# Optimization experiments

Hardware: AMD Instinct MI355X
Metric: run time of the kernel (lower is better)

The kernel has to match this reference:

```python
import jax, jax.numpy as jnp
import numpy as np

HIDDEN = 1024
NUM_CLASSES = 10
NUM_GAUSSIANS = 8
IN_FEATURES = 16
HEADS = NUM_CLASSES * NUM_GAUSSIANS * IN_FEATURES * 2  # 2560 tiny Linear(hidden,1) heads


def setup_inputs() -> dict:
    key = jax.random.key(0)
    kx, kw, kb = jax.random.split(key, 3)
    x = jax.random.normal(kx, (8192, HIDDEN), dtype=jnp.float32)
    # Stacked weights of the 2560 per-head Linear(hidden,1) layers.
    bound = 1.0 / np.sqrt(HIDDEN)
    W = jax.random.uniform(kw, (HIDDEN, HEADS), minval=-bound, maxval=bound, dtype=jnp.float32)
    b = jax.random.uniform(kb, (HEADS,), minval=-bound, maxval=bound, dtype=jnp.float32)
    return {"x": x, "W": W, "b": b}


def reference(x, W, b):
    batch = x.shape[0]
    # Fused form of the Python loop of Linear(hidden,1)+Sigmoid per head.
    z = jax.nn.sigmoid(x @ W + b)  # [batch, HEADS]
    return z.reshape(batch, NUM_CLASSES, NUM_GAUSSIANS, IN_FEATURES, 2)
```

## Files before the change

### kernel.cpp

```cpp
#include <hip/hip_runtime.h>
#include <hip/hip_bf16.h>

#define HIDDEN 1024
#define HEADS  2560

#define BM 256
#define BN 128
#define BK 32
#define NT (HIDDEN / BK)
#define ABYT (BM * BK * 2)
#define BBYT (BN * BK * 2)
#define BUFSZ (ABYT + BBYT)

typedef float  f32x4  __attribute__((ext_vector_type(4)));
typedef __bf16 bf16x8 __attribute__((ext_vector_type(8)));
typedef __bf16 bf16x4 __attribute__((ext_vector_type(4)));

__device__ __forceinline__ void gload_lds16(const void* g, void* l) {
    __builtin_amdgcn_global_load_lds(
        (const __attribute__((address_space(1))) unsigned int*)g,
        (__attribute__((address_space(3))) unsigned int*)l, 16, 0, 0);
}
__device__ __forceinline__ unsigned swz(unsigned x) {
    return x ^ (((x >> 6) & 3u) << 4);
}

__global__ __launch_bounds__(256)
void cvt_all(const float* __restrict__ x, const float* __restrict__ W,
             __bf16* __restrict__ xc, __bf16* __restrict__ Wt, int n8)
{
    if (blockIdx.x < 640) {
        __shared__ __bf16 tile[64][72];
        const int t  = threadIdx.x;
        const int n0 = (blockIdx.x % 40) * 64;
        const int k0 = (blockIdx.x / 40) * 64;

        #pragma unroll
        for (int i = 0; i < 4; ++i) {
            const int k    = (t >> 4) + i * 16;
            const int col4 = (t & 15) * 4;
            const float4 v = *reinterpret_cast<const float4*>(
                W + (size_t)(k0 + k) * HEADS + n0 + col4);
            bf16x4 h;
            h[0] = (__bf16)v.x; h[1] = (__bf16)v.y; h[2] = (__bf16)v.z; h[3] = (__bf16)v.w;
            *reinterpret_cast<bf16x4*>(&tile[k][col4]) = h;
        }
        __syncthreads();
        #pragma unroll
        for (int i = 0; i < 4; ++i) {
            const int n  = (t >> 4) + i * 16;
            const int k4 = (t & 15) * 4;
            bf16x4 h;
            h[0] = tile[k4 + 0][n]; h[1] = tile[k4 + 1][n];
            h[2] = tile[k4 + 2][n]; h[3] = tile[k4 + 3][n];
            *reinterpret_cast<bf16x4*>(Wt + (size_t)(n0 + n) * HIDDEN + k0 + k4) = h;
        }
    } else {
        int idx    = (blockIdx.x - 640) * blockDim.x + threadIdx.x;
        int stride = (gridDim.x - 640) * blockDim.x;
        for (int i = idx; i < n8; i += stride) {
            const float4 a = *reinterpret_cast<const float4*>(x + (size_t)i * 8);
            const float4 b = *reinterpret_cast<const float4*>(x + (size_t)i * 8 + 4);
            bf16x8 h;
            h[0] = (__bf16)a.x; h[1] = (__bf16)a.y; h[2] = (__bf16)a.z; h[3] = (__bf16)a.w;
            h[4] = (__bf16)b.x; h[5] = (__bf16)b.y; h[6] = (__bf16)b.z; h[7] = (__bf16)b.w;
            *reinterpret_cast<bf16x8*>(xc + (size_t)i * 8) = h;
        }
    }
}

__global__ __launch_bounds__(512, 4)
void gemm_sq(const __bf16* __restrict__ A, const __bf16* __restrict__ Bt,
             const float* __restrict__ bias, float* __restrict__ out)
{
    __shared__ char lds[2 * BUFSZ];

    const int t    = threadIdx.x;
    const int lane = t & 63;
    const int w    = t >> 6;
    const int wr   = w & 3;
    const int wc   = w >> 2;
    const int lhi  = lane >> 4;
    const int llo  = lane & 15;

    const int g   = (blockIdx.x & 7) * 80 + (blockIdx.x >> 3);
    const int bx  = g / 20;
    const int by  = g % 20;
    const int bm0 = bx * BM;
    const int bn0 = by * BN;

    const unsigned d0 = (unsigned)(t * 16);
    const unsigned r0 = d0 >> 6;
    const unsigned c0 = (d0 & 63) ^ ((r0 & 3u) << 4);
    const char* asrc0 = (const char*)A  + (size_t)(bm0 + r0) * (HIDDEN * 2) + c0;
    const char* bsrc0 = (const char*)Bt + (size_t)(bn0 + r0) * (HIDDEN * 2) + c0;
    char* adst0 = (char*)lds + d0;
    char* bdst0 = (char*)lds + ABYT + d0;

    const unsigned klo  = ((unsigned)(lhi * 16)) ^ ((unsigned)((llo & 3) << 4));
    const unsigned rowA = (unsigned)((wr * 64 + llo) * 64);
    const unsigned rowB = (unsigned)ABYT + (unsigned)((wc * 64 + llo) * 64);

    f32x4 acc[4][4];
    #pragma unroll
    for (int m = 0; m < 4; ++m)
        #pragma unroll
        for (int n = 0; n < 4; ++n)
            acc[m][n] = f32x4{0.f, 0.f, 0.f, 0.f};

    gload_lds16(asrc0,          adst0);
    gload_lds16(asrc0 + 262144, adst0 + 8192);
    gload_lds16(bsrc0,          bdst0);
    asm volatile("s_waitcnt vmcnt(0)" ::: "memory");
    __builtin_amdgcn_s_barrier();

    for (int k = 0; k < NT; ++k) {
        const char* buf  = lds + (k & 1) * BUFSZ;
        const unsigned nb = (unsigned)(((k + 1) & 1) * BUFSZ);
        const int   koff = (k + 1) * 64;

        if (k + 1 < NT) {
            gload_lds16(asrc0 + koff,          adst0 + nb);
            gload_lds16(asrc0 + koff + 262144, adst0 + nb + 8192);
            gload_lds16(bsrc0 + koff,          bdst0 + nb);
        }

        bf16x8 af[4], bfr[4];
        #pragma unroll
        for (int m = 0; m < 4; ++m)
            af[m]  = *(const bf16x8*)(buf + rowA + m * 1024 + klo);
        #pragma unroll
        for (int n = 0; n < 4; ++n)
            bfr[n] = *(const bf16x8*)(buf + rowB + n * 1024 + klo);
        #pragma unroll
        for (int m = 0; m < 4; ++m)
            #pragma unroll
            for (int n = 0; n < 4; ++n)
                acc[m][n] = __builtin_amdgcn_mfma_f32_16x16x32_bf16(
                    af[m], bfr[n], acc[m][n], 0, 0, 0);

        asm volatile("s_waitcnt vmcnt(0)" ::: "memory");
        __builtin_amdgcn_s_barrier();
    }

    #pragma unroll
    for (int n = 0; n < 4; ++n) {
        const int col  = bn0 + wc * 64 + n * 16 + llo;
        const float bv = bias[col];
        #pragma unroll
        for (int m = 0; m < 4; ++m) {
            const int row0 = bm0 + wr * 64 + m * 16 + lhi * 4;
            #pragma unroll
            for (int r = 0; r < 4; ++r) {
                const float z = acc[m][n][r] + bv;
                out[(size_t)(row0 + r) * HEADS + col] = __fdividef(1.0f, 1.0f + __expf(-z));
            }
        }
    }
}

#define FBM 128
#define FBN 128
#define FBK 32
#define FLDK 40

__global__ __launch_bounds__(256)
void lch_gemm(const float* __restrict__ x, const float* __restrict__ W,
              const float* __restrict__ b, float* __restrict__ out)
{
    __shared__ __bf16 As[FBM][FLDK];
    __shared__ __bf16 Bs[FBN][FLDK];

    const int t   = threadIdx.x;
    const int bm0 = blockIdx.x * FBM;
    const int bn0 = blockIdx.y * FBN;
    const int lane = t & 63;
    const int wid  = t >> 6;
    const int wr   = wid >> 1;
    const int wc   = wid & 1;
    const int lhi  = lane >> 4;
    const int llo  = lane & 15;

    f32x4 acc[4][4];
    #pragma unroll
    for (int i = 0; i < 4; ++i)
        #pragma unroll
        for (int j = 0; j < 4; ++j)
            acc[i][j] = f32x4{0.f, 0.f, 0.f, 0.f};

    const int bn_col  = t & 127;
    const int bk_base = (t >> 7) * 16;

    for (int k0 = 0; k0 < HIDDEN; k0 += FBK) {
        #pragma unroll
        for (int i = 0; i < 4; ++i) {
            const int f   = t + i * 256;
            const int row = f >> 3;
            const int c4  = (f & 7) * 4;
            const float4 v = *reinterpret_cast<const float4*>(
                x + (size_t)(bm0 + row) * HIDDEN + k0 + c4);
            bf16x4 h;
            h[0] = (__bf16)v.x; h[1] = (__bf16)v.y;
            h[2] = (__bf16)v.z; h[3] = (__bf16)v.w;
            *reinterpret_cast<bf16x4*>(&As[row][c4]) = h;
        }
        {
            const float* wp = W + (size_t)(k0 + bk_base) * HEADS + bn0 + bn_col;
            bf16x8 h0, h1;
            #pragma unroll
            for (int i = 0; i < 8; ++i) h0[i] = (__bf16)wp[(size_t)i * HEADS];
            #pragma unroll
            for (int i = 0; i < 8; ++i) h1[i] = (__bf16)wp[(size_t)(i + 8) * HEADS];
            *reinterpret_cast<bf16x8*>(&Bs[bn_col][bk_base])     = h0;
            *reinterpret_cast<bf16x8*>(&Bs[bn_col][bk_base + 8]) = h1;
        }
        __syncthreads();

        bf16x8 af[4], bfr[4];
        #pragma unroll
        for (int i = 0; i < 4; ++i)
            af[i] = *reinterpret_cast<const bf16x8*>(&As[wr * 64 + i * 16 + llo][lhi * 8]);
        #pragma unroll
        for (int j = 0; j < 4; ++j)
            bfr[j] = *reinterpret_cast<const bf16x8*>(&Bs[wc * 64 + j * 16 + llo][lhi * 8]);
        #pragma unroll
        for (int i = 0; i < 4; ++i)
            #pragma unroll
            for (int j = 0; j < 4; ++j)
                acc[i][j] = __builtin_amdgcn_mfma_f32_16x16x32_bf16(
                    af[i], bfr[j], acc[i][j], 0, 0, 0);
        __syncthreads();
    }

    #pragma unroll
    for (int j = 0; j < 4; ++j) {
        const int col  = bn0 + wc * 64 + j * 16 + llo;
        const float bv = b[col];
        #pragma unroll
        for (int i = 0; i < 4; ++i) {
            const int row0 = bm0 + wr * 64 + i * 16 + lhi * 4;
            #pragma unroll
            for (int r = 0; r < 4; ++r) {
                const float z = acc[i][j][r] + bv;
                out[(size_t)(row0 + r) * HEADS + col] = 1.0f / (1.0f + __expf(-z));
            }
        }
    }
}

extern "C" void kernel_launch(void* const* d_in, const int* in_sizes, int n_in,
                              void* d_out, int out_size, void* d_ws, size_t ws_size,
                              hipStream_t stream) {
    const float* x = (const float*)d_in[0];
    const float* W = (const float*)d_in[1];
    const float* b = (const float*)d_in[2];
    float* out     = (float*)d_out;

    const int M = in_sizes[0] / HIDDEN;

    const size_t xc_bytes = (size_t)M * HIDDEN * sizeof(__bf16);
    const size_t wt_bytes = (size_t)HEADS * HIDDEN * sizeof(__bf16);

    if (ws_size >= xc_bytes + wt_bytes && (M % BM) == 0) {
        __bf16* xc = (__bf16*)d_ws;
        __bf16* Wt = (__bf16*)((char*)d_ws + xc_bytes);

        cvt_all<<<640 + 2048, 256, 0, stream>>>(x, W, xc, Wt, M * HIDDEN / 8);

        const int nwg = (M / BM) * (HEADS / BN);
        gemm_sq<<<nwg, 512, 0, stream>>>(xc, Wt, b, out);
    } else {
        dim3 grid(M / FBM, HEADS / FBN);
        lch_gemm<<<grid, dim3(256), 0, stream>>>(x, W, b, out);
    }
}
```

Baseline: 81.20 us.

## Widen GEMM N-tile to 160 and switch to paired-row 128-byte LDS swizzle

Raises the block N tile from 128 to 160, so each wave computes a 4x5 grid of MFMA tiles. The grid becomes 32x16=512 workgroups, which divides evenly across the 8-way XCD remap instead of 640. The LDS layout is reorganised so two 64-byte K rows share one 128-byte line with a 3-bit XOR swizzle, aimed at reducing bank conflicts. An extra tail load by 128 threads fills the added B rows. More accumulators raise register pressure under the 4-waves launch bound, and the extra tail load adds per-iteration imbalance.

```diff
diff --git a/kernel.cpp b/kernel.cpp
--- a/kernel.cpp
+++ b/kernel.cpp
@@ -5,7 +5,7 @@
 #define HEADS  2560
 
 #define BM 256
-#define BN 128
+#define BN 160
 #define BK 32
 #define NT (HIDDEN / BK)
 #define ABYT (BM * BK * 2)
@@ -20,9 +20,6 @@
     __builtin_amdgcn_global_load_lds(
         (const __attribute__((address_space(1))) unsigned int*)g,
         (__attribute__((address_space(3))) unsigned int*)l, 16, 0, 0);
-}
-__device__ __forceinline__ unsigned swz(unsigned x) {
-    return x ^ (((x >> 6) & 3u) << 4);
 }
 
 __global__ __launch_bounds__(256)
@@ -70,7 +67,7 @@
 }
 
 __global__ __launch_bounds__(512, 4)
-void gemm_sq(const __bf16* __restrict__ A, const __bf16* __restrict__ Bt,
+void gemm_pp(const __bf16* __restrict__ A, const __bf16* __restrict__ Bt,
              const float* __restrict__ bias, float* __restrict__ out)
 {
     __shared__ char lds[2 * BUFSZ];
@@ -83,34 +80,47 @@
     const int lhi  = lane >> 4;
     const int llo  = lane & 15;
 
-    const int g   = (blockIdx.x & 7) * 80 + (blockIdx.x >> 3);
-    const int bx  = g / 20;
-    const int by  = g % 20;
+    const int g   = (blockIdx.x & 7) * 64 + (blockIdx.x >> 3);
+    const int bx  = g >> 4;
+    const int by  = g & 15;
     const int bm0 = bx * BM;
     const int bn0 = by * BN;
 
-    const unsigned d0 = (unsigned)(t * 16);
-    const unsigned r0 = d0 >> 6;
-    const unsigned c0 = (d0 & 63) ^ ((r0 & 3u) << 4);
-    const char* asrc0 = (const char*)A  + (size_t)(bm0 + r0) * (HIDDEN * 2) + c0;
-    const char* bsrc0 = (const char*)Bt + (size_t)(bn0 + r0) * (HIDDEN * 2) + c0;
-    char* adst0 = (char*)lds + d0;
-    char* bdst0 = (char*)lds + ABYT + d0;
-
-    const unsigned klo  = ((unsigned)(lhi * 16)) ^ ((unsigned)((llo & 3) << 4));
-    const unsigned rowA = (unsigned)((wr * 64 + llo) * 64);
-    const unsigned rowB = (unsigned)ABYT + (unsigned)((wc * 64 + llo) * 64);
-
-    f32x4 acc[4][4];
+    const unsigned dA = (unsigned)(t * 16);
+    unsigned prowA = dA >> 7;
+    unsigned ilA   = (dA & 127u) ^ ((prowA & 7u) << 4);
+    const char* asrc0 = (const char*)A
+        + (size_t)(bm0 + (int)((prowA << 1) | (ilA >> 6))) * 2048 + (ilA & 63u);
+    const char* bsrc0 = (const char*)Bt
+        + (size_t)(bn0 + (int)((prowA << 1) | (ilA >> 6))) * 2048 + (ilA & 63u);
+    char* adst0 = (char*)lds + dA;
+    char* bdst0 = (char*)lds + ABYT + dA;
+
+    const unsigned dBt = 8192u + (unsigned)((t & 127) * 16);
+    unsigned prowT = dBt >> 7;
+    unsigned ilT   = (dBt & 127u) ^ ((prowT & 7u) << 4);
+    const char* bsrct = (const char*)Bt
+        + (size_t)(bn0 + (int)((prowT << 1) | (ilT >> 6))) * 2048 + (ilT & 63u);
+    char* bdstt = (char*)lds + ABYT + dBt;
+    const bool tail = (t < 128);
+
+    const unsigned klo = (unsigned)(((llo & 1) << 6) | (lhi << 4))
+                       ^ (unsigned)(((llo >> 1) & 7) << 4);
+    const unsigned laneR = (unsigned)((llo >> 1) * 128);
+    const unsigned baseA = (unsigned)(wr * 4096) + laneR;
+    const unsigned baseB = (unsigned)ABYT + (unsigned)(wc * 5120) + laneR;
+
+    f32x4 acc[4][5];
     #pragma unroll
     for (int m = 0; m < 4; ++m)
         #pragma unroll
-        for (int n = 0; n < 4; ++n)
+        for (int n = 0; n < 5; ++n)
             acc[m][n] = f32x4{0.f, 0.f, 0.f, 0.f};
 
     gload_lds16(asrc0,          adst0);
     gload_lds16(asrc0 + 262144, adst0 + 8192);
     gload_lds16(bsrc0,          bdst0);
+    if (tail) gload_lds16(bsrct, bdstt);
     asm volatile("s_waitcnt vmcnt(0)" ::: "memory");
     __builtin_amdgcn_s_barrier();
 
@@ -123,19 +133,20 @@
             gload_lds16(asrc0 + koff,          adst0 + nb);
             gload_lds16(asrc0 + koff + 262144, adst0 + nb + 8192);
             gload_lds16(bsrc0 + koff,          bdst0 + nb);
-        }
-
-        bf16x8 af[4], bfr[4];
+            if (tail) gload_lds16(bsrct + koff, bdstt + nb);
+        }
+
+        bf16x8 af[4], bfr[5];
         #pragma unroll
         for (int m = 0; m < 4; ++m)
-            af[m]  = *(const bf16x8*)(buf + rowA + m * 1024 + klo);
-        #pragma unroll
-        for (int n = 0; n < 4; ++n)
-            bfr[n] = *(const bf16x8*)(buf + rowB + n * 1024 + klo);
+            af[m]  = *(const bf16x8*)(buf + baseA + m * 1024 + klo);
+        #pragma unroll
+        for (int n = 0; n < 5; ++n)
+            bfr[n] = *(const bf16x8*)(buf + baseB + n * 1024 + klo);
         #pragma unroll
         for (int m = 0; m < 4; ++m)
             #pragma unroll
-            for (int n = 0; n < 4; ++n)
+            for (int n = 0; n < 5; ++n)
                 acc[m][n] = __builtin_amdgcn_mfma_f32_16x16x32_bf16(
                     af[m], bfr[n], acc[m][n], 0, 0, 0);
 
@@ -144,8 +155,8 @@
     }
 
     #pragma unroll
-    for (int n = 0; n < 4; ++n) {
-        const int col  = bn0 + wc * 64 + n * 16 + llo;
+    for (int n = 0; n < 5; ++n) {
+        const int col  = bn0 + wc * 80 + n * 16 + llo;
         const float bv = bias[col];
         #pragma unroll
         for (int m = 0; m < 4; ++m) {
@@ -268,7 +279,7 @@
         cvt_all<<<640 + 2048, 256, 0, stream>>>(x, W, xc, Wt, M * HIDDEN / 8);
 
         const int nwg = (M / BM) * (HEADS / BN);
-        gemm_sq<<<nwg, 512, 0, stream>>>(xc, Wt, b, out);
+        gemm_pp<<<nwg, 512, 0, stream>>>(xc, Wt, b, out);
     } else {
         dim3 grid(M / FBM, HEADS / FBN);
         lch_gemm<<<grid, dim3(256), 0, stream>>>(x, W, b, out);
```

After: 70.09 us. -13.7%, faster.

## Triple-buffer LDS in bf16 GEMM with prefetch distance two and new swizzle

Applied to the files above, without the earlier changes.

Moves the GEMM main loop from double to triple buffering in LDS. Loads for tile k+2 are issued while tile k is computed, and each iteration waits only for the older batch (vmcnt(3)), so more global-load latency is hidden. The LDS layout also changes from 64-byte rows with a 4-way XOR to 128-byte paired rows with an 8-way XOR swizzle, meant to cut bank conflicts on the fragment reads. LDS use per block goes up by half, which may limit how many blocks fit on a CU.

```diff
diff --git a/kernel.cpp b/kernel.cpp
--- a/kernel.cpp
+++ b/kernel.cpp
@@ -20,9 +20,6 @@
     __builtin_amdgcn_global_load_lds(
         (const __attribute__((address_space(1))) unsigned int*)g,
         (__attribute__((address_space(3))) unsigned int*)l, 16, 0, 0);
-}
-__device__ __forceinline__ unsigned swz(unsigned x) {
-    return x ^ (((x >> 6) & 3u) << 4);
 }
 
 __global__ __launch_bounds__(256)
@@ -70,10 +67,10 @@
 }
 
 __global__ __launch_bounds__(512, 4)
-void gemm_sq(const __bf16* __restrict__ A, const __bf16* __restrict__ Bt,
+void gemm_r3(const __bf16* __restrict__ A, const __bf16* __restrict__ Bt,
              const float* __restrict__ bias, float* __restrict__ out)
 {
-    __shared__ char lds[2 * BUFSZ];
+    __shared__ char lds[3 * BUFSZ];
 
     const int t    = threadIdx.x;
     const int lane = t & 63;
@@ -89,17 +86,21 @@
     const int bm0 = bx * BM;
     const int bn0 = by * BN;
 
-    const unsigned d0 = (unsigned)(t * 16);
-    const unsigned r0 = d0 >> 6;
-    const unsigned c0 = (d0 & 63) ^ ((r0 & 3u) << 4);
-    const char* asrc0 = (const char*)A  + (size_t)(bm0 + r0) * (HIDDEN * 2) + c0;
-    const char* bsrc0 = (const char*)Bt + (size_t)(bn0 + r0) * (HIDDEN * 2) + c0;
-    char* adst0 = (char*)lds + d0;
-    char* bdst0 = (char*)lds + ABYT + d0;
-
-    const unsigned klo  = ((unsigned)(lhi * 16)) ^ ((unsigned)((llo & 3) << 4));
-    const unsigned rowA = (unsigned)((wr * 64 + llo) * 64);
-    const unsigned rowB = (unsigned)ABYT + (unsigned)((wc * 64 + llo) * 64);
+    const unsigned dA = (unsigned)(t * 16);
+    {
+    }
+    const unsigned prowA = dA >> 7;
+    const unsigned ilA   = (dA & 127u) ^ ((prowA & 7u) << 4);
+    const char* asrc0 = (const char*)A
+        + (size_t)(bm0 + (int)((prowA << 1) | (ilA >> 6))) * 2048 + (ilA & 63u);
+    const char* bsrc0 = (const char*)Bt
+        + (size_t)(bn0 + (int)((prowA << 1) | (ilA >> 6))) * 2048 + (ilA & 63u);
+
+    const unsigned klo = (unsigned)(((llo & 1) << 6) | (lhi << 4))
+                       ^ (unsigned)(((llo >> 1) & 7) << 4);
+    const unsigned laneR = (unsigned)((llo >> 1) * 128);
+    const unsigned baseA = (unsigned)(wr * 4096) + laneR;
+    const unsigned baseB = (unsigned)ABYT + (unsigned)(wc * 4096) + laneR;
 
     f32x4 acc[4][4];
     #pragma unroll
@@ -108,30 +109,37 @@
         for (int n = 0; n < 4; ++n)
             acc[m][n] = f32x4{0.f, 0.f, 0.f, 0.f};
 
-    gload_lds16(asrc0,          adst0);
-    gload_lds16(asrc0 + 262144, adst0 + 8192);
-    gload_lds16(bsrc0,          bdst0);
-    asm volatile("s_waitcnt vmcnt(0)" ::: "memory");
+    char* const lb = (char*)lds;
+
+    gload_lds16(asrc0,               lb + dA);
+    gload_lds16(asrc0 + 262144,      lb + dA + 8192);
+    gload_lds16(bsrc0,               lb + ABYT + dA);
+    gload_lds16(asrc0 + 64,          lb + BUFSZ + dA);
+    gload_lds16(asrc0 + 64 + 262144, lb + BUFSZ + dA + 8192);
+    gload_lds16(bsrc0 + 64,          lb + BUFSZ + ABYT + dA);
+    asm volatile("s_waitcnt vmcnt(3)" ::: "memory");
     __builtin_amdgcn_s_barrier();
 
+    int bi = 0;
+    int si = 2;
     for (int k = 0; k < NT; ++k) {
-        const char* buf  = lds + (k & 1) * BUFSZ;
-        const unsigned nb = (unsigned)(((k + 1) & 1) * BUFSZ);
-        const int   koff = (k + 1) * 64;
-
-        if (k + 1 < NT) {
-            gload_lds16(asrc0 + koff,          adst0 + nb);
-            gload_lds16(asrc0 + koff + 262144, adst0 + nb + 8192);
-            gload_lds16(bsrc0 + koff,          bdst0 + nb);
+        const char* buf = lb + bi * BUFSZ;
+
+        if (k + 2 < NT) {
+            char* nbf = lb + si * BUFSZ;
+            const int koff = (k + 2) * 64;
+            gload_lds16(asrc0 + koff,          nbf + dA);
+            gload_lds16(asrc0 + koff + 262144, nbf + dA + 8192);
+            gload_lds16(bsrc0 + koff,          nbf + ABYT + dA);
         }
 
         bf16x8 af[4], bfr[4];
         #pragma unroll
         for (int m = 0; m < 4; ++m)
-            af[m]  = *(const bf16x8*)(buf + rowA + m * 1024 + klo);
+            af[m]  = *(const bf16x8*)(buf + baseA + m * 1024 + klo);
         #pragma unroll
         for (int n = 0; n < 4; ++n)
-            bfr[n] = *(const bf16x8*)(buf + rowB + n * 1024 + klo);
+            bfr[n] = *(const bf16x8*)(buf + baseB + n * 1024 + klo);
         #pragma unroll
         for (int m = 0; m < 4; ++m)
             #pragma unroll
@@ -139,8 +147,12 @@
                 acc[m][n] = __builtin_amdgcn_mfma_f32_16x16x32_bf16(
                     af[m], bfr[n], acc[m][n], 0, 0, 0);
 
-        asm volatile("s_waitcnt vmcnt(0)" ::: "memory");
+        if (k < NT - 2) asm volatile("s_waitcnt vmcnt(3)" ::: "memory");
+        else            asm volatile("s_waitcnt vmcnt(0)" ::: "memory");
         __builtin_amdgcn_s_barrier();
+
+        bi = (bi == 2) ? 0 : bi + 1;
+        si = (si == 2) ? 0 : si + 1;
     }
 
     #pragma unroll
@@ -268,7 +280,7 @@
         cvt_all<<<640 + 2048, 256, 0, stream>>>(x, W, xc, Wt, M * HIDDEN / 8);
 
         const int nwg = (M / BM) * (HEADS / BN);
-        gemm_sq<<<nwg, 512, 0, stream>>>(xc, Wt, b, out);
+        gemm_r3<<<nwg, 512, 0, stream>>>(xc, Wt, b, out);
     } else {
         dim3 grid(M / FBM, HEADS / FBN);
         lch_gemm<<<grid, dim3(256), 0, stream>>>(x, W, b, out);
```

Result: faster. 76.56 us (-5.7%).
